# Kernel tuning notes

Hardware: AMD Instinct MI355X
Metric: run time of the kernel (lower is better)

The kernel has to match this reference:

```python
import jax, jax.numpy as jnp
import numpy as np

N = 8192
IN_F = 256
OUT_F = 256


def setup_inputs() -> dict:
    key = jax.random.key(0)
    k_v, k_adj, k1, k2, k3, kb = jax.random.split(key, 6)
    stdv = 1.0 / np.sqrt(OUT_F)
    V = jax.random.normal(k_v, (N, IN_F), dtype=jnp.float32)
    adj = jax.random.randint(k_adj, (N, N), 0, 4, dtype=jnp.int32)
    w1 = jax.random.uniform(k1, (IN_F, OUT_F), jnp.float32, -stdv, stdv)
    w2 = jax.random.uniform(k2, (IN_F, OUT_F), jnp.float32, -stdv, stdv)
    w3 = jax.random.uniform(k3, (IN_F, OUT_F), jnp.float32, -stdv, stdv)
    bias = jax.random.uniform(kb, (OUT_F,), jnp.float32, -stdv, stdv)
    return {"V": V, "adj": adj, "w1": w1, "w2": w2, "w3": w3, "bias": bias}


def reference(V, adj, w1, w2, w3, bias):
    # typed relational GCN: for each edge type k in {1,2,3},
    # aggregate (adj==k) @ (V @ wk), then sum and add bias
    o1 = jnp.matmul((adj == 1).astype(jnp.float32), jnp.matmul(V, w1))
    o2 = jnp.matmul((adj == 2).astype(jnp.float32), jnp.matmul(V, w2))
    o3 = jnp.matmul((adj == 3).astype(jnp.float32), jnp.matmul(V, w3))
    return o1 + o2 + o3 + bias
```

## Files before the change

kernel.cpp:

```cpp
#include <hip/hip_runtime.h>

typedef __attribute__((ext_vector_type(4))) float f32x4;
typedef __attribute__((ext_vector_type(16))) float f32x16;
typedef __attribute__((ext_vector_type(4))) unsigned short u16x4;
typedef __attribute__((ext_vector_type(4))) int i32x4;
typedef __attribute__((ext_vector_type(8))) __bf16 bf16x8;

union FragAB {
  u16x4 u[2];
  i32x4 v;
  bf16x8 f;
};

static __device__ __forceinline__ unsigned short f2bf(float x) {
  union { float f; unsigned u; } v;
  v.f = x;
  unsigned r = v.u + 0x7FFFu + ((v.u >> 16) & 1u);
  return (unsigned short)(r >> 16);
}

#define NN 8192

__global__ __launch_bounds__(256) void k_bias(const float* __restrict__ bias,
                                              float* __restrict__ out) {
  out[(size_t)blockIdx.x * 256 + threadIdx.x] = bias[threadIdx.x];
}

__global__ __launch_bounds__(256) void k_transform(
    const float* __restrict__ V, const float* __restrict__ w1,
    const float* __restrict__ w2, const float* __restrict__ w3,
    unsigned short* __restrict__ Bp) {
  int bx = blockIdx.x;
  int rb = bx & 63;
  int nb = bx >> 6;
  const float* W = (nb < 4) ? w1 : (nb < 8) ? w2 : w3;
  int nc0 = (nb & 3) * 64;
  int tid = threadIdx.x;
  int lane = tid & 63;
  int wv = tid >> 6;
  int wm = wv >> 1, wn = wv & 1;
  int q = lane >> 4, l16 = lane & 15;

  __shared__ unsigned short tA[128][36];
  __shared__ unsigned short tB[64][36];

  f32x4 acc[4][2];
#pragma unroll
  for (int i = 0; i < 4; i++)
#pragma unroll
    for (int j = 0; j < 2; j++) acc[i][j] = (f32x4)0.0f;

  for (int kk = 0; kk < 256; kk += 32) {
    {
      int r = tid >> 1, c0 = (tid & 1) * 16;
      const float* src = V + (size_t)(rb * 128 + r) * 256 + kk + c0;
      f32x4 f0 = *(const f32x4*)(src + 0);
      f32x4 f1 = *(const f32x4*)(src + 4);
      f32x4 f2 = *(const f32x4*)(src + 8);
      f32x4 f3 = *(const f32x4*)(src + 12);
      unsigned short* d = &tA[r][c0];
      d[0] = f2bf(f0.x);  d[1] = f2bf(f0.y);  d[2] = f2bf(f0.z);  d[3] = f2bf(f0.w);
      d[4] = f2bf(f1.x);  d[5] = f2bf(f1.y);  d[6] = f2bf(f1.z);  d[7] = f2bf(f1.w);
      d[8] = f2bf(f2.x);  d[9] = f2bf(f2.y);  d[10] = f2bf(f2.z); d[11] = f2bf(f2.w);
      d[12] = f2bf(f3.x); d[13] = f2bf(f3.y); d[14] = f2bf(f3.z); d[15] = f2bf(f3.w);
    }
    {
      int r = tid >> 3, c0 = (tid & 7) * 8;
      const float* src = W + (size_t)(kk + r) * 256 + nc0 + c0;
      f32x4 g0 = *(const f32x4*)(src);
      f32x4 g1 = *(const f32x4*)(src + 4);
      tB[c0 + 0][r] = f2bf(g0.x); tB[c0 + 1][r] = f2bf(g0.y);
      tB[c0 + 2][r] = f2bf(g0.z); tB[c0 + 3][r] = f2bf(g0.w);
      tB[c0 + 4][r] = f2bf(g1.x); tB[c0 + 5][r] = f2bf(g1.y);
      tB[c0 + 6][r] = f2bf(g1.z); tB[c0 + 7][r] = f2bf(g1.w);
    }
    __syncthreads();
    FragAB af[4], bf[2];
#pragma unroll
    for (int mt = 0; mt < 4; mt++) {
      const unsigned short* p = &tA[wm * 64 + mt * 16 + l16][q * 8];
      af[mt].u[0] = *(const u16x4*)p;
      af[mt].u[1] = *(const u16x4*)(p + 4);
    }
#pragma unroll
    for (int nt = 0; nt < 2; nt++) {
      const unsigned short* p = &tB[wn * 32 + nt * 16 + l16][q * 8];
      bf[nt].u[0] = *(const u16x4*)p;
      bf[nt].u[1] = *(const u16x4*)(p + 4);
    }
#pragma unroll
    for (int mt = 0; mt < 4; mt++)
#pragma unroll
      for (int nt = 0; nt < 2; nt++)
        acc[mt][nt] = __builtin_amdgcn_mfma_f32_16x16x32_bf16(
            af[mt].f, bf[nt].f, acc[mt][nt], 0, 0, 0);
    __syncthreads();
  }
  int ty = nb >> 2;
#pragma unroll
  for (int mt = 0; mt < 4; mt++)
#pragma unroll
    for (int nt = 0; nt < 2; nt++) {
      int n = (nb & 3) * 64 + wn * 32 + nt * 16 + l16;
      int j0 = rb * 128 + wm * 64 + mt * 16 + q * 4;
      u16x4 hv;
      hv.x = f2bf(acc[mt][nt].x);
      hv.y = f2bf(acc[mt][nt].y);
      hv.z = f2bf(acc[mt][nt].z);
      hv.w = f2bf(acc[mt][nt].w);
      size_t idx = (size_t)ty * 2097152 + (size_t)(j0 >> 4) * 4096 + n * 16 + (j0 & 15);
      *(u16x4*)(Bp + idx) = hv;
    }
}

__global__ __launch_bounds__(256) void k_agg(const int* __restrict__ adj,
                                             const unsigned short* __restrict__ Bp,
                                             float* __restrict__ out) {
  int bx = blockIdx.x;
  int ks = bx & 3, rb = bx >> 2;
  int tid = threadIdx.x, lane = tid & 63;
  int wv = tid >> 6;
  int q = lane >> 5, l32 = lane & 31;

  __shared__ __align__(16) int smem[16384];
  int* wbase = smem + wv * 4096;

  f32x16 acc[2][2];
  acc[0][0] = (f32x16)0.0f;
  acc[0][1] = (f32x16)0.0f;
  acc[1][0] = (f32x16)0.0f;
  acc[1][1] = (f32x16)0.0f;

  const int* ast = adj + (size_t)(rb * 64 + (lane >> 3)) * NN + ks * 2048 + (lane & 7) * 4;
  int swzw = (((lane & 7) ^ ((lane >> 3) & 7)) * 4);
  int wrow = (lane >> 3) * 32;
  int sw7 = l32 & 7;

  const unsigned short* bb[3][2];
#pragma unroll
  for (int ty = 0; ty < 3; ty++)
#pragma unroll
    for (int nt = 0; nt < 2; nt++) {
      int n = wv * 64 + nt * 32 + l32;
      bb[ty][nt] = Bp + (size_t)ty * 2097152 + (size_t)ks * 524288 + n * 16 + q * 8;
    }

  i32x4 st[8];
#pragma unroll
  for (int j = 0; j < 8; j++) st[j] = *(const i32x4*)(ast + j * 8 * NN);
#pragma unroll
  for (int j = 0; j < 8; j++)
    *(i32x4*)(wbase + j * 256 + wrow + swzw) = st[j];
#pragma unroll
  for (int j = 0; j < 8; j++) st[j] = *(const i32x4*)(ast + j * 8 * NN + 32);

  for (int s = 0; s < 64; s++) {
    int bufoff = (s & 1) * 2048;
    FragAB bv[2][3][2];
    size_t soff = (size_t)s * 8192;
#pragma unroll
    for (int kh = 0; kh < 2; kh++)
#pragma unroll
      for (int ty = 0; ty < 3; ty++)
#pragma unroll
        for (int nt = 0; nt < 2; nt++)
          bv[kh][ty][nt].v = *(const i32x4*)(bb[ty][nt] + soff + kh * 4096);

#pragma unroll
    for (int kh = 0; kh < 2; kh++)
#pragma unroll
      for (int mt = 0; mt < 2; mt++) {
        int rowoff = bufoff + mt * 1024 + l32 * 32;
        int c0 = kh * 4 + q * 2;
        i32x4 e0 = *(const i32x4*)(wbase + rowoff + ((c0 ^ sw7) * 4));
        i32x4 e1 = *(const i32x4*)(wbase + rowoff + (((c0 + 1) ^ sw7) * 4));
#pragma unroll
        for (int ty = 0; ty < 3; ty++) {
          FragAB af;
          u16x4 lo, hi;
          int t = ty + 1;
          lo.x = (e0.x == t) ? 0x3F80 : 0;
          lo.y = (e0.y == t) ? 0x3F80 : 0;
          lo.z = (e0.z == t) ? 0x3F80 : 0;
          lo.w = (e0.w == t) ? 0x3F80 : 0;
          hi.x = (e1.x == t) ? 0x3F80 : 0;
          hi.y = (e1.y == t) ? 0x3F80 : 0;
          hi.z = (e1.z == t) ? 0x3F80 : 0;
          hi.w = (e1.w == t) ? 0x3F80 : 0;
          af.u[0] = lo;
          af.u[1] = hi;
          acc[mt][0] = __builtin_amdgcn_mfma_f32_32x32x16_bf16(
              af.f, bv[kh][ty][0].f, acc[mt][0], 0, 0, 0);
          acc[mt][1] = __builtin_amdgcn_mfma_f32_32x32x16_bf16(
              af.f, bv[kh][ty][1].f, acc[mt][1], 0, 0, 0);
        }
      }

    if (s < 63) {
      int obuf = bufoff ^ 2048;
#pragma unroll
      for (int j = 0; j < 8; j++)
        *(i32x4*)(wbase + obuf + j * 256 + wrow + swzw) = st[j];
      if (s < 62) {
        const int* anext = ast + (s + 2) * 32;
#pragma unroll
        for (int j = 0; j < 8; j++) st[j] = *(const i32x4*)(anext + j * 8 * NN);
      }
    }
  }

#pragma unroll
  for (int mt = 0; mt < 2; mt++)
#pragma unroll
    for (int nt = 0; nt < 2; nt++) {
      int colbase = wv * 64 + nt * 32 + l32;
      int rowb = rb * 64 + mt * 32 + 4 * q;
#pragma unroll
      for (int r = 0; r < 16; r++) {
        int row = rowb + (r & 3) + 8 * (r >> 2);
        atomicAdd(out + (size_t)row * 256 + colbase, acc[mt][nt][r]);
      }
    }
}

extern "C" void kernel_launch(void* const* d_in, const int* in_sizes, int n_in,
                              void* d_out, int out_size, void* d_ws,
                              size_t ws_size, hipStream_t stream) {
  const float* V = (const float*)d_in[0];
  const int* adj = (const int*)d_in[1];
  const float* w1 = (const float*)d_in[2];
  const float* w2 = (const float*)d_in[3];
  const float* w3 = (const float*)d_in[4];
  const float* bias = (const float*)d_in[5];
  float* out = (float*)d_out;
  unsigned short* Bp = (unsigned short*)d_ws;

  k_bias<<<dim3(NN), dim3(256), 0, stream>>>(bias, out);
  k_transform<<<dim3(768), dim3(256), 0, stream>>>(V, w1, w2, w3, Bp);
  k_agg<<<dim3(512), dim3(256), 0, stream>>>(adj, Bp, out);
}
```

Before: 490.0 us.

## Pack adjacency into 2-bit codes and use bit-plane decomposition for edge types

```diff
diff --git a/kernel.cpp b/kernel.cpp
--- a/kernel.cpp
+++ b/kernel.cpp
@@ -17,6 +17,11 @@
   v.f = x;
   unsigned r = v.u + 0x7FFFu + ((v.u >> 16) & 1u);
   return (unsigned short)(r >> 16);
+}
+static __device__ __forceinline__ float b2f(unsigned short u) {
+  union { unsigned u; float f; } v;
+  v.u = ((unsigned)u) << 16;
+  return v.f;
 }
 
 #define NN 8192
@@ -113,17 +118,71 @@
     }
 }
 
-__global__ __launch_bounds__(256) void k_agg(const int* __restrict__ adj,
+__global__ __launch_bounds__(256) void k_fix(unsigned short* __restrict__ Bp) {
+  size_t i = ((size_t)blockIdx.x * 256 + threadIdx.x) * 8;
+  union { i32x4 v; unsigned short s[8]; } a, b, c, r;
+  a.v = *(const i32x4*)(Bp + i);
+  b.v = *(const i32x4*)(Bp + 2097152 + i);
+  c.v = *(const i32x4*)(Bp + 4194304 + i);
+#pragma unroll
+  for (int e = 0; e < 8; e++)
+    r.s[e] = f2bf(b2f(c.s[e]) - b2f(a.s[e]) - b2f(b.s[e]));
+  *(i32x4*)(Bp + 4194304 + i) = r.v;
+}
+
+__global__ __launch_bounds__(256) void k_pack(const int* __restrict__ adj,
+                                              unsigned* __restrict__ P) {
+  int bx = blockIdx.x;
+  int rowblk = bx >> 3, ks = bx & 7;
+  int t = threadIdx.x;
+  int r0 = rowblk * 64;
+  __shared__ unsigned hal[64][129];
+
+  for (int p = 0; p < 32; p++) {
+    int rl = p * 2 + (t >> 7);
+    int o = t & 127;
+    const int* src = adj + (size_t)(r0 + rl) * NN + ks * 1024 + o * 8;
+    i32x4 v0 = *(const i32x4*)src;
+    i32x4 v1 = *(const i32x4*)(src + 4);
+    unsigned b = (unsigned)(v0.x & 3) | ((unsigned)(v0.y & 3) << 2) |
+                 ((unsigned)(v0.z & 3) << 4) | ((unsigned)(v0.w & 3) << 6) |
+                 ((unsigned)(v1.x & 3) << 8) | ((unsigned)(v1.y & 3) << 10) |
+                 ((unsigned)(v1.z & 3) << 12) | ((unsigned)(v1.w & 3) << 14);
+    hal[rl][o] = b;
+  }
+  __syncthreads();
+  for (int i = 0; i < 16; i++) {
+    int oi = i * 256 + t;
+    int row = oi & 63, sq = oi >> 6;
+    int s = sq >> 1, q = sq & 1;
+    unsigned lo = hal[row][s * 4 + q];
+    unsigned hi = hal[row][s * 4 + 2 + q];
+    P[((size_t)(ks * 32 + s) * 2 + q) * 8192 + r0 + row] = lo | (hi << 16);
+  }
+}
+
+static __device__ __forceinline__ void expand2(unsigned bits, FragAB& fA,
+                                               FragAB& fB) {
+  unsigned short a[8], b[8];
+#pragma unroll
+  for (int e = 0; e < 8; e++) {
+    a[e] = (bits & (1u << (2 * e))) ? 0x3F80 : 0;
+    b[e] = (bits & (2u << (2 * e))) ? 0x3F80 : 0;
+  }
+  fA.u[0] = u16x4{a[0], a[1], a[2], a[3]};
+  fA.u[1] = u16x4{a[4], a[5], a[6], a[7]};
+  fB.u[0] = u16x4{b[0], b[1], b[2], b[3]};
+  fB.u[1] = u16x4{b[4], b[5], b[6], b[7]};
+}
+
+__global__ __launch_bounds__(256) void k_agg(const unsigned* __restrict__ P,
                                              const unsigned short* __restrict__ Bp,
                                              float* __restrict__ out) {
   int bx = blockIdx.x;
-  int ks = bx & 3, rb = bx >> 2;
+  int ks = bx & 7, rb = bx >> 3;
   int tid = threadIdx.x, lane = tid & 63;
   int wv = tid >> 6;
   int q = lane >> 5, l32 = lane & 31;
-
-  __shared__ __align__(16) int smem[16384];
-  int* wbase = smem + wv * 4096;
 
   f32x16 acc[2][2];
   acc[0][0] = (f32x16)0.0f;
@@ -131,10 +190,7 @@
   acc[1][0] = (f32x16)0.0f;
   acc[1][1] = (f32x16)0.0f;
 
-  const int* ast = adj + (size_t)(rb * 64 + (lane >> 3)) * NN + ks * 2048 + (lane & 7) * 4;
-  int swzw = (((lane & 7) ^ ((lane >> 3) & 7)) * 4);
-  int wrow = (lane >> 3) * 32;
-  int sw7 = l32 & 7;
+  const unsigned* pp = P + ((size_t)ks * 64 + q) * 8192 + rb * 64 + l32;
 
   const unsigned short* bb[3][2];
 #pragma unroll
@@ -142,20 +198,12 @@
 #pragma unroll
     for (int nt = 0; nt < 2; nt++) {
       int n = wv * 64 + nt * 32 + l32;
-      bb[ty][nt] = Bp + (size_t)ty * 2097152 + (size_t)ks * 524288 + n * 16 + q * 8;
-    }
-
-  i32x4 st[8];
-#pragma unroll
-  for (int j = 0; j < 8; j++) st[j] = *(const i32x4*)(ast + j * 8 * NN);
-#pragma unroll
-  for (int j = 0; j < 8; j++)
-    *(i32x4*)(wbase + j * 256 + wrow + swzw) = st[j];
-#pragma unroll
-  for (int j = 0; j < 8; j++) st[j] = *(const i32x4*)(ast + j * 8 * NN + 32);
-
-  for (int s = 0; s < 64; s++) {
-    int bufoff = (s & 1) * 2048;
+      bb[ty][nt] = Bp + (size_t)ty * 2097152 + (size_t)ks * 262144 + n * 16 + q * 8;
+    }
+
+  unsigned pk0 = pp[0], pk1 = pp[32];
+
+  for (int s = 0; s < 32; s++) {
     FragAB bv[2][3][2];
     size_t soff = (size_t)s * 8192;
 #pragma unroll
@@ -165,48 +213,36 @@
 #pragma unroll
         for (int nt = 0; nt < 2; nt++)
           bv[kh][ty][nt].v = *(const i32x4*)(bb[ty][nt] + soff + kh * 4096);
-
-#pragma unroll
-    for (int kh = 0; kh < 2; kh++)
-#pragma unroll
-      for (int mt = 0; mt < 2; mt++) {
-        int rowoff = bufoff + mt * 1024 + l32 * 32;
-        int c0 = kh * 4 + q * 2;
-        i32x4 e0 = *(const i32x4*)(wbase + rowoff + ((c0 ^ sw7) * 4));
-        i32x4 e1 = *(const i32x4*)(wbase + rowoff + (((c0 + 1) ^ sw7) * 4));
-#pragma unroll
-        for (int ty = 0; ty < 3; ty++) {
-          FragAB af;
-          u16x4 lo, hi;
-          int t = ty + 1;
-          lo.x = (e0.x == t) ? 0x3F80 : 0;
-          lo.y = (e0.y == t) ? 0x3F80 : 0;
-          lo.z = (e0.z == t) ? 0x3F80 : 0;
-          lo.w = (e0.w == t) ? 0x3F80 : 0;
-          hi.x = (e1.x == t) ? 0x3F80 : 0;
-          hi.y = (e1.y == t) ? 0x3F80 : 0;
-          hi.z = (e1.z == t) ? 0x3F80 : 0;
-          hi.w = (e1.w == t) ? 0x3F80 : 0;
-          af.u[0] = lo;
-          af.u[1] = hi;
-          acc[mt][0] = __builtin_amdgcn_mfma_f32_32x32x16_bf16(
-              af.f, bv[kh][ty][0].f, acc[mt][0], 0, 0, 0);
-          acc[mt][1] = __builtin_amdgcn_mfma_f32_32x32x16_bf16(
-              af.f, bv[kh][ty][1].f, acc[mt][1], 0, 0, 0);
-        }
+    unsigned npk0 = 0, npk1 = 0;
+    if (s < 31) {
+      npk0 = pp[(s + 1) * 16384];
+      npk1 = pp[(s + 1) * 16384 + 32];
+    }
+#pragma unroll
+    for (int mt = 0; mt < 2; mt++) {
+      unsigned pw = mt ? pk1 : pk0;
+#pragma unroll
+      for (int kh = 0; kh < 2; kh++) {
+        unsigned bits = (pw >> (kh * 16)) & 0xFFFFu;
+        FragAB fA, fB, fC;
+        expand2(bits, fA, fB);
+        fC.v = fA.v & fB.v;
+        acc[mt][0] = __builtin_amdgcn_mfma_f32_32x32x16_bf16(
+            fA.f, bv[kh][0][0].f, acc[mt][0], 0, 0, 0);
+        acc[mt][1] = __builtin_amdgcn_mfma_f32_32x32x16_bf16(
+            fA.f, bv[kh][0][1].f, acc[mt][1], 0, 0, 0);
+        acc[mt][0] = __builtin_amdgcn_mfma_f32_32x32x16_bf16(
+            fB.f, bv[kh][1][0].f, acc[mt][0], 0, 0, 0);
+        acc[mt][1] = __builtin_amdgcn_mfma_f32_32x32x16_bf16(
+            fB.f, bv[kh][1][1].f, acc[mt][1], 0, 0, 0);
+        acc[mt][0] = __builtin_amdgcn_mfma_f32_32x32x16_bf16(
+            fC.f, bv[kh][2][0].f, acc[mt][0], 0, 0, 0);
+        acc[mt][1] = __builtin_amdgcn_mfma_f32_32x32x16_bf16(
+            fC.f, bv[kh][2][1].f, acc[mt][1], 0, 0, 0);
       }
-
-    if (s < 63) {
-      int obuf = bufoff ^ 2048;
-#pragma unroll
-      for (int j = 0; j < 8; j++)
-        *(i32x4*)(wbase + obuf + j * 256 + wrow + swzw) = st[j];
-      if (s < 62) {
-        const int* anext = ast + (s + 2) * 32;
-#pragma unroll
-        for (int j = 0; j < 8; j++) st[j] = *(const i32x4*)(anext + j * 8 * NN);
-      }
-    }
+    }
+    pk0 = npk0;
+    pk1 = npk1;
   }
 
 #pragma unroll
@@ -234,8 +270,11 @@
   const float* bias = (const float*)d_in[5];
   float* out = (float*)d_out;
   unsigned short* Bp = (unsigned short*)d_ws;
+  unsigned* P = (unsigned*)((char*)d_ws + 12582912);
 
   k_bias<<<dim3(NN), dim3(256), 0, stream>>>(bias, out);
+  k_pack<<<dim3(1024), dim3(256), 0, stream>>>(adj, P);
   k_transform<<<dim3(768), dim3(256), 0, stream>>>(V, w1, w2, w3, Bp);
-  k_agg<<<dim3(512), dim3(256), 0, stream>>>(adj, Bp, out);
-}
+  k_fix<<<dim3(1024), dim3(256), 0, stream>>>(Bp);
+  k_agg<<<dim3(1024), dim3(256), 0, stream>>>(P, Bp, out);
+}
```

New measurement: 523.1 us. 1.07x slower.
